# Kernel tuning notes

Measured on AMD Instinct MI355X. Metric: run time of the kernel, lower is better.

Reference implementation:

```python
import jax, jax.numpy as jnp
import numpy as np

B, C, T = 8, 128, 4096
H = C // 2  # 64


def setup_inputs() -> dict:
    key = jax.random.key(0)
    ks = jax.random.split(key, 9)
    s = 1.0 / np.sqrt(C)
    so = 1.0 / np.sqrt(H)
    return {
        "x": jax.random.normal(ks[0], (B, C, T), dtype=jnp.float32),
        "w_theta": jax.random.normal(ks[1], (H, C), dtype=jnp.float32) * s,
        "b_theta": jax.random.normal(ks[2], (H,), dtype=jnp.float32) * s,
        "w_phi": jax.random.normal(ks[3], (H, C), dtype=jnp.float32) * s,
        "b_phi": jax.random.normal(ks[4], (H,), dtype=jnp.float32) * s,
        "w_g": jax.random.normal(ks[5], (H, C), dtype=jnp.float32) * s,
        "b_g": jax.random.normal(ks[6], (H,), dtype=jnp.float32) * s,
        "w_out": jax.random.normal(ks[7], (C, H), dtype=jnp.float32) * so,
        "b_out": jax.random.normal(ks[8], (C,), dtype=jnp.float32) * so,
    }


def reference(x, w_theta, b_theta, w_phi, b_phi, w_g, b_g, w_out, b_out):
    # 1x1 conv == channel-mixing linear: [B,C,T] -> [B,H,T]
    theta = jnp.einsum("hc,bct->bht", w_theta, x) + b_theta[None, :, None]
    phi = jnp.einsum("hc,bct->bht", w_phi, x) + b_phi[None, :, None]
    g = jnp.einsum("hc,bct->bht", w_g, x) + b_g[None, :, None]
    # scores[b,t,s] = theta[b,:,t] . phi[b,:,s]; softmax over s (last dim)
    scores = jnp.einsum("bht,bhs->bts", theta, phi)  # [B,T,T]
    attn = jax.nn.softmax(scores, axis=-1)
    # out[b,h,t] = sum_s g[b,h,s] * attn[b,t,s]
    out = jnp.einsum("bhs,bts->bht", g, attn)  # [B,H,T]
    out = jnp.einsum("ch,bht->bct", w_out, out) + b_out[None, :, None]
    return x + out
```

## Files before the change

kernel.cpp:

```cpp
#include <hip/hip_runtime.h>
#include <hip/hip_bf16.h>

typedef _Float16 half_t;
typedef half_t halfx8 __attribute__((ext_vector_type(8)));
typedef half_t halfx4 __attribute__((ext_vector_type(4)));
typedef half_t halfx2 __attribute__((ext_vector_type(2)));
typedef __fp16 fp16x2 __attribute__((ext_vector_type(2)));
typedef float f32x4 __attribute__((ext_vector_type(4)));
typedef float f32x16 __attribute__((ext_vector_type(16)));
typedef int i32x4 __attribute__((ext_vector_type(4)));

#define B_ 8
#define C_ 128
#define T_ 4096
#define H_ 64
#define L2E 1.44269504088896340736f

static __device__ __forceinline__ halfx2 pk2(float a, float b) {
    fp16x2 r = __builtin_amdgcn_cvt_pkrtz(a, b);
    return __builtin_bit_cast(halfx2, r);
}
static __device__ __forceinline__ int pk2i(float a, float b) {
    return __builtin_bit_cast(int, __builtin_amdgcn_cvt_pkrtz(a, b));
}
static __device__ __forceinline__ float fast_exp2(float x) {
    return __builtin_amdgcn_exp2f(x);
}
static __device__ __forceinline__ float max3f(float a, float b, float c) {
    return fmaxf(fmaxf(a, b), c);
}
static __device__ __forceinline__ int swz(int row, int col) {
    return (row << 6) + (col ^ ((row & 7) << 3));
}
static __device__ __forceinline__ int swz4(int row, int col) {
    return (row << 6) + ((col & ~7) ^ ((row & 7) << 3)) + (col & 7);
}

__global__ __launch_bounds__(256) void proj_kernel(
    const float* __restrict__ x,
    const float* __restrict__ w_theta, const float* __restrict__ b_theta,
    const float* __restrict__ w_phi,   const float* __restrict__ b_phi,
    const float* __restrict__ w_g,     const float* __restrict__ b_g,
    half_t* __restrict__ Q, half_t* __restrict__ Ko, half_t* __restrict__ Vt)
{
    __shared__ __align__(16) half_t xt[64][136];
    __shared__ __align__(16) half_t ts[64][72];

    const int tid  = threadIdx.x;
    const int lane = tid & 63;
    const int wave = tid >> 6;
    const int b    = blockIdx.x >> 6;
    const int t0   = (blockIdx.x & 63) << 6;

    const int rowA  = lane & 15;
    const int kgrp  = lane >> 4;
    const int row_d = kgrp << 2;

    const float* xb = x + (size_t)b * C_ * T_ + t0;
    #pragma unroll
    for (int it = 0; it < 8; ++it) {
        int li = it * 256 + tid;
        int c  = li >> 4;
        int tc = li & 15;
        f32x4 v = *(const f32x4*)(xb + (size_t)c * T_ + tc * 4);
        #pragma unroll
        for (int j = 0; j < 4; ++j) xt[tc * 4 + j][c] = (half_t)v[j];
    }

    const int h0 = wave << 4;
    const float* Ws[3] = {w_theta, w_phi, w_g};
    const float* Bs[3] = {b_theta, b_phi, b_g};
    halfx8 wa[3][4];
    #pragma unroll
    for (int m = 0; m < 3; ++m) {
        const float* wrow = Ws[m] + (size_t)(h0 + rowA) * C_;
        #pragma unroll
        for (int cc = 0; cc < 4; ++cc) {
            const float* p = wrow + cc * 32 + kgrp * 8;
            f32x4 a = *(const f32x4*)p;
            f32x4 c2 = *(const f32x4*)(p + 4);
            halfx8 f;
            f[0]=(half_t)a[0]; f[1]=(half_t)a[1]; f[2]=(half_t)a[2]; f[3]=(half_t)a[3];
            f[4]=(half_t)c2[0];f[5]=(half_t)c2[1];f[6]=(half_t)c2[2];f[7]=(half_t)c2[3];
            wa[m][cc] = f;
        }
    }

    __syncthreads();

    #pragma unroll
    for (int m = 0; m < 3; ++m) {
        f32x4 acc[4] = {};
        #pragma unroll
        for (int tt = 0; tt < 4; ++tt) {
            #pragma unroll
            for (int cc = 0; cc < 4; ++cc) {
                halfx8 bfrag = *(const halfx8*)&xt[tt * 16 + rowA][cc * 32 + kgrp * 8];
                acc[tt] = __builtin_amdgcn_mfma_f32_16x16x32_f16(wa[m][cc], bfrag, acc[tt], 0, 0, 0);
            }
        }
        float bias[4];
        #pragma unroll
        for (int r = 0; r < 4; ++r) bias[r] = Bs[m][h0 + row_d + r];

        if (m < 2) {
            const float sc = (m == 0) ? L2E : 1.0f;
            #pragma unroll
            for (int tt = 0; tt < 4; ++tt)
                #pragma unroll
                for (int r = 0; r < 4; ++r)
                    ts[tt * 16 + rowA][h0 + row_d + r] = (half_t)((acc[tt][r] + bias[r]) * sc);
            __syncthreads();
            half_t* dst = (m == 0 ? Q : Ko) + ((size_t)b * T_ + t0) * H_;
            #pragma unroll
            for (int it = 0; it < 2; ++it) {
                int q = it * 256 + tid;
                int t = q >> 3, hc = q & 7;
                *(halfx8*)(dst + (size_t)t * H_ + hc * 8) = *(const halfx8*)&ts[t][hc * 8];
            }
            __syncthreads();
        } else {
            half_t* dst = Vt + (size_t)b * H_ * T_ + t0;
            #pragma unroll
            for (int tt = 0; tt < 4; ++tt)
                #pragma unroll
                for (int r = 0; r < 4; ++r)
                    dst[(size_t)(h0 + row_d + r) * T_ + tt * 16 + rowA] = (half_t)(acc[tt][r] + bias[r]);
        }
    }
}

__global__ __launch_bounds__(256, 4) void attn_kernel(
    const half_t* __restrict__ Q, const half_t* __restrict__ K,
    const half_t* __restrict__ Vt, half_t* __restrict__ Op,
    float* __restrict__ Mp, float* __restrict__ Lp, int NS)
{
    __shared__ __align__(16) half_t Ks[2][64 * 64];
    __shared__ __align__(16) half_t Vs[2][64 * 64];

    const int tid  = threadIdx.x;
    const int wave = tid >> 6;
    const int lane = tid & 63;
    const int qb   = blockIdx.x / NS;
    const int sp   = blockIdx.x - qb * NS;
    const int b    = qb >> 5;
    const int t0   = (qb & 31) << 7;
    const int q0   = t0 + wave * 32;
    const int lq   = lane & 31;
    const int hi   = lane >> 5;
    const int NT   = T_ / (64 * NS);
    const int sbase = sp * (T_ / NS);

    halfx8 qf[4];
    const half_t* qr = Q + ((size_t)b * T_ + q0 + lq) * H_ + hi * 8;
    #pragma unroll
    for (int kc = 0; kc < 4; ++kc) qf[kc] = *(const halfx8*)(qr + kc * 16);

    f32x16 oacc[2] = {};
    float mr = -INFINITY, lr = 0.f;

    const int r0 = tid >> 3;
    const int c8 = (tid & 7) * 8;
    const int gA = (c8 & ~15) + ((c8 & 8) >> 1);
    const half_t* kp = K  + (size_t)b * T_ * H_ + (size_t)(sbase + r0) * H_ + c8;
    const half_t* vp = Vt + (size_t)b * H_ * T_ + (size_t)r0 * T_ + sbase + c8;

    halfx8 rK0 = *(const halfx8*)kp;
    halfx8 rK1 = *(const halfx8*)(kp + 32 * H_);
    halfx8 rV0 = *(const halfx8*)vp;
    halfx8 rV1 = *(const halfx8*)(vp + 32 * T_);
    kp += 64 * H_; vp += 64;

    {
        *(halfx8*)&Ks[0][swz(r0, c8)]      = rK0;
        *(halfx8*)&Ks[0][swz(r0 + 32, c8)] = rK1;
        union { halfx8 h8; halfx4 h4[2]; } u0, u1;
        u0.h8 = rV0; u1.h8 = rV1;
        *(halfx4*)&Vs[0][swz4(r0, gA)]          = u0.h4[0];
        *(halfx4*)&Vs[0][swz4(r0, gA + 8)]      = u0.h4[1];
        *(halfx4*)&Vs[0][swz4(r0 + 32, gA)]     = u1.h4[0];
        *(halfx4*)&Vs[0][swz4(r0 + 32, gA + 8)] = u1.h4[1];
    }
    __syncthreads();

    for (int t = 0; t < NT; ++t) {
        const int cur = t & 1;
        const bool more = (t + 1 < NT);
        if (more) {
            rK0 = *(const halfx8*)kp;
            rK1 = *(const halfx8*)(kp + 32 * H_);
            rV0 = *(const halfx8*)vp;
            rV1 = *(const halfx8*)(vp + 32 * T_);
            kp += 64 * H_; vp += 64;
        }

        f32x16 sacc[2] = {};
        __builtin_amdgcn_s_setprio(1);
        #pragma unroll
        for (int st = 0; st < 2; ++st)
            #pragma unroll
            for (int kc = 0; kc < 4; ++kc) {
                halfx8 kf = *(const halfx8*)&Ks[cur][swz(st * 32 + lq, kc * 16 + hi * 8)];
                sacc[st] = __builtin_amdgcn_mfma_f32_32x32x16_f16(kf, qf[kc], sacc[st], 0, 0, 0);
            }
        __builtin_amdgcn_s_setprio(0);

        float pm;
        {
            float a0 = max3f(sacc[0][0],  sacc[0][1],  sacc[0][2]);
            float a1 = max3f(sacc[0][3],  sacc[0][4],  sacc[0][5]);
            float a2 = max3f(sacc[0][6],  sacc[0][7],  sacc[0][8]);
            float a3 = max3f(sacc[0][9],  sacc[0][10], sacc[0][11]);
            float a4 = max3f(sacc[0][12], sacc[0][13], sacc[0][14]);
            float b0 = max3f(sacc[1][0],  sacc[1][1],  sacc[1][2]);
            float b1 = max3f(sacc[1][3],  sacc[1][4],  sacc[1][5]);
            float b2 = max3f(sacc[1][6],  sacc[1][7],  sacc[1][8]);
            float b3 = max3f(sacc[1][9],  sacc[1][10], sacc[1][11]);
            float b4 = max3f(sacc[1][12], sacc[1][13], sacc[1][14]);
            float c0 = max3f(a0, a1, sacc[0][15]);
            float c1 = max3f(a2, a3, a4);
            float c2 = max3f(b0, b1, sacc[1][15]);
            float c3 = max3f(b2, b3, b4);
            pm = fmaxf(max3f(c0, c1, c2), c3);
        }
        if (__any(pm > mr + 8.f)) {
            pm = fmaxf(pm, __shfl_xor(pm, 32));
            float mnew  = fmaxf(mr, pm);
            float scale = fast_exp2(mr - mnew);
            mr = mnew; lr *= scale;
            #pragma unroll
            for (int dt = 0; dt < 2; ++dt)
                #pragma unroll
                for (int r = 0; r < 16; ++r) oacc[dt][r] *= scale;
        }
        float p0 = 0.f, p1 = 0.f, p2 = 0.f, p3 = 0.f;
        #pragma unroll
        for (int st = 0; st < 2; ++st) {
            #pragma unroll
            for (int r = 0; r < 16; r += 4) {
                float e0 = fast_exp2(sacc[st][r + 0] - mr);
                float e1 = fast_exp2(sacc[st][r + 1] - mr);
                float e2 = fast_exp2(sacc[st][r + 2] - mr);
                float e3 = fast_exp2(sacc[st][r + 3] - mr);
                sacc[st][r + 0] = e0; sacc[st][r + 1] = e1;
                sacc[st][r + 2] = e2; sacc[st][r + 3] = e3;
                p0 += e0; p1 += e1; p2 += e2; p3 += e3;
            }
        }
        float ps = (p0 + p1) + (p2 + p3);
        lr += ps + __shfl_xor(ps, 32);

        halfx8 pfrag[4];
        #pragma unroll
        for (int sc = 0; sc < 4; ++sc) {
            const int st = sc >> 1, rb = (sc & 1) * 8;
            i32x4 w;
            w[0] = pk2i(sacc[st][rb + 0], sacc[st][rb + 1]);
            w[1] = pk2i(sacc[st][rb + 2], sacc[st][rb + 3]);
            w[2] = pk2i(sacc[st][rb + 4], sacc[st][rb + 5]);
            w[3] = pk2i(sacc[st][rb + 6], sacc[st][rb + 7]);
            pfrag[sc] = __builtin_bit_cast(halfx8, w);
        }

        __builtin_amdgcn_s_setprio(1);
        #pragma unroll
        for (int sc = 0; sc < 4; ++sc) {
            halfx8 vf0 = *(const halfx8*)&Vs[cur][swz(lq,      sc * 16 + hi * 8)];
            halfx8 vf1 = *(const halfx8*)&Vs[cur][swz(32 + lq, sc * 16 + hi * 8)];
            oacc[0] = __builtin_amdgcn_mfma_f32_32x32x16_f16(vf0, pfrag[sc], oacc[0], 0, 0, 0);
            oacc[1] = __builtin_amdgcn_mfma_f32_32x32x16_f16(vf1, pfrag[sc], oacc[1], 0, 0, 0);
        }
        __builtin_amdgcn_s_setprio(0);

        if (more) {
            const int nxt = cur ^ 1;
            *(halfx8*)&Ks[nxt][swz(r0, c8)]      = rK0;
            *(halfx8*)&Ks[nxt][swz(r0 + 32, c8)] = rK1;
            union { halfx8 h8; halfx4 h4[2]; } u0, u1;
            u0.h8 = rV0; u1.h8 = rV1;
            *(halfx4*)&Vs[nxt][swz4(r0, gA)]          = u0.h4[0];
            *(halfx4*)&Vs[nxt][swz4(r0, gA + 8)]      = u0.h4[1];
            *(halfx4*)&Vs[nxt][swz4(r0 + 32, gA)]     = u1.h4[0];
            *(halfx4*)&Vs[nxt][swz4(r0 + 32, gA + 8)] = u1.h4[1];
            __syncthreads();
        }
    }

    const int BT = B_ * T_;
    const int grow = b * T_ + q0 + lq;
    float inv = 1.f / lr;
    half_t* od = Op + ((size_t)sp * BT + grow) * H_;
    #pragma unroll
    for (int dt = 0; dt < 2; ++dt)
        #pragma unroll
        for (int g = 0; g < 4; ++g) {
            union { halfx2 h2[2]; halfx4 h4; } u;
            u.h2[0] = pk2(oacc[dt][g * 4 + 0] * inv, oacc[dt][g * 4 + 1] * inv);
            u.h2[1] = pk2(oacc[dt][g * 4 + 2] * inv, oacc[dt][g * 4 + 3] * inv);
            *(halfx4*)(od + dt * 32 + g * 8 + hi * 4) = u.h4;
        }
    if (Mp != nullptr && hi == 0) {
        Mp[(size_t)sp * BT + grow] = mr;
        Lp[(size_t)sp * BT + grow] = lr;
    }
}

__global__ __launch_bounds__(256) void merge_kernel(
    const half_t* __restrict__ Op, const float* __restrict__ Mp,
    const float* __restrict__ Lp, half_t* __restrict__ O, int NS)
{
    const int idx = blockIdx.x * 256 + threadIdx.x;
    const int row = idx >> 3;
    const int hc  = (idx & 7) * 8;
    const int BT  = B_ * T_;

    float m = -INFINITY;
    for (int s = 0; s < NS; ++s) m = fmaxf(m, Mp[(size_t)s * BT + row]);
    float W = 0.f;
    float acc[8] = {};
    for (int s = 0; s < NS; ++s) {
        float w = Lp[(size_t)s * BT + row] * __builtin_amdgcn_exp2f(Mp[(size_t)s * BT + row] - m);
        W += w;
        halfx8 o = *(const halfx8*)(Op + ((size_t)s * BT + row) * H_ + hc);
        #pragma unroll
        for (int j = 0; j < 8; ++j) acc[j] += w * (float)o[j];
    }
    float inv = 1.f / W;
    halfx8 r;
    #pragma unroll
    for (int j = 0; j < 8; ++j) r[j] = (half_t)(acc[j] * inv);
    *(halfx8*)(O + (size_t)row * H_ + hc) = r;
}

__global__ __launch_bounds__(256) void outproj_kernel(
    const half_t* __restrict__ O, const float* __restrict__ w_out,
    const float* __restrict__ b_out, const float* __restrict__ x,
    float* __restrict__ out)
{
    __shared__ __align__(16) half_t Ot[64][72];

    const int tid  = threadIdx.x;
    const int lane = tid & 63;
    const int wave = tid >> 6;
    const int b    = blockIdx.x >> 6;
    const int t0   = (blockIdx.x & 63) << 6;

    const int rowA  = lane & 15;
    const int kgrp  = lane >> 4;
    const int row_d = kgrp << 2;

    #pragma unroll
    for (int it = 0; it < 2; ++it) {
        int q = it * 256 + tid;
        int t = q >> 3, hc = q & 7;
        *(halfx8*)&Ot[t][hc * 8] = *(const halfx8*)(O + ((size_t)b * T_ + t0 + t) * H_ + hc * 8);
    }

    const int c0 = wave * 32;
    halfx8 wf[2][2];
    #pragma unroll
    for (int ct = 0; ct < 2; ++ct) {
        const float* wrow = w_out + (size_t)(c0 + ct * 16 + rowA) * H_;
        #pragma unroll
        for (int hc = 0; hc < 2; ++hc) {
            const float* p = wrow + hc * 32 + kgrp * 8;
            f32x4 a = *(const f32x4*)p;
            f32x4 c2 = *(const f32x4*)(p + 4);
            halfx8 f;
            f[0]=(half_t)a[0]; f[1]=(half_t)a[1]; f[2]=(half_t)a[2]; f[3]=(half_t)a[3];
            f[4]=(half_t)c2[0];f[5]=(half_t)c2[1];f[6]=(half_t)c2[2];f[7]=(half_t)c2[3];
            wf[ct][hc] = f;
        }
    }

    __syncthreads();

    #pragma unroll
    for (int ct = 0; ct < 2; ++ct) {
        #pragma unroll
        for (int tt = 0; tt < 4; ++tt) {
            f32x4 acc = {};
            #pragma unroll
            for (int hc = 0; hc < 2; ++hc) {
                halfx8 of = *(const halfx8*)&Ot[tt * 16 + rowA][hc * 32 + kgrp * 8];
                acc = __builtin_amdgcn_mfma_f32_16x16x32_f16(wf[ct][hc], of, acc, 0, 0, 0);
            }
            const int c = c0 + ct * 16 + row_d;
            const size_t base = (size_t)b * C_ * T_ + t0 + tt * 16 + rowA;
            #pragma unroll
            for (int r = 0; r < 4; ++r) {
                size_t idx = base + (size_t)(c + r) * T_;
                out[idx] = x[idx] + b_out[c + r] + acc[r];
            }
        }
    }
}

extern "C" void kernel_launch(void* const* d_in, const int* in_sizes, int n_in,
                              void* d_out, int out_size, void* d_ws, size_t ws_size,
                              hipStream_t stream) {
    const float* x       = (const float*)d_in[0];
    const float* w_theta = (const float*)d_in[1];
    const float* b_theta = (const float*)d_in[2];
    const float* w_phi   = (const float*)d_in[3];
    const float* b_phi   = (const float*)d_in[4];
    const float* w_g     = (const float*)d_in[5];
    const float* b_g     = (const float*)d_in[6];
    const float* w_out   = (const float*)d_in[7];
    const float* b_out   = (const float*)d_in[8];
    float* out = (float*)d_out;

    const size_t mat = (size_t)B_ * T_ * H_;
    const size_t BT  = (size_t)B_ * T_;
    half_t* Qw = (half_t*)d_ws;
    half_t* Kw = Qw + mat;
    half_t* Vw = Kw + mat;
    half_t* Ow = Vw + mat;
    const size_t base_b = 4 * mat * sizeof(half_t);

    auto need = [&](size_t ns) { return base_b + ns * mat * 2 + ns * BT * 8; };
    const int NS = (ws_size >= need(4)) ? 4 : ((ws_size >= need(2)) ? 2 : 1);

    half_t* Opart = Ow;
    float*  Mp = nullptr;
    float*  Lp = nullptr;
    if (NS > 1) {
        Opart = (half_t*)((char*)d_ws + base_b);
        Mp = (float*)((char*)d_ws + base_b + (size_t)NS * mat * 2);
        Lp = Mp + (size_t)NS * BT;
    }

    proj_kernel<<<dim3(B_ * (T_ / 64)), dim3(256), 0, stream>>>(
        x, w_theta, b_theta, w_phi, b_phi, w_g, b_g, Qw, Kw, Vw);
    attn_kernel<<<dim3(B_ * (T_ / 128) * NS), dim3(256), 0, stream>>>(
        Qw, Kw, Vw, Opart, Mp, Lp, NS);
    if (NS > 1)
        merge_kernel<<<dim3((int)(BT * H_ / (256 * 8))), dim3(256), 0, stream>>>(
            Opart, Mp, Lp, Ow, NS);
    outproj_kernel<<<dim3(B_ * (T_ / 64)), dim3(256), 0, stream>>>(Ow, w_out, b_out, x, out);
}
```

Measured before the change: 77.41 us.

## Fuse split-KV merge into output projection and defer row-sum shuffle

The separate merge kernel that combines split-KV partial outputs is removed. That combine now runs inside the output-projection kernel while it loads its tile into shared memory, which saves a launch and a round trip of the merged O through global memory. The cross-half row-sum shuffle in the attention inner loop is also moved out to a single shuffle after the loop, cutting one cross-lane operation per iteration. The trade-off is that the outproj load phase does more scattered reads and some scalar math before its MFMA work.

```diff
diff --git a/kernel.cpp b/kernel.cpp
--- a/kernel.cpp
+++ b/kernel.cpp
@@ -247,8 +247,7 @@
                 p0 += e0; p1 += e1; p2 += e2; p3 += e3;
             }
         }
-        float ps = (p0 + p1) + (p2 + p3);
-        lr += ps + __shfl_xor(ps, 32);
+        lr += (p0 + p1) + (p2 + p3);
 
         halfx8 pfrag[4];
         #pragma unroll
@@ -288,7 +287,8 @@
 
     const int BT = B_ * T_;
     const int grow = b * T_ + q0 + lq;
-    float inv = 1.f / lr;
+    const float lrt = lr + __shfl_xor(lr, 32);
+    float inv = 1.f / lrt;
     half_t* od = Op + ((size_t)sp * BT + grow) * H_;
     #pragma unroll
     for (int dt = 0; dt < 2; ++dt)
@@ -301,41 +301,15 @@
         }
     if (Mp != nullptr && hi == 0) {
         Mp[(size_t)sp * BT + grow] = mr;
-        Lp[(size_t)sp * BT + grow] = lr;
-    }
-}
-
-__global__ __launch_bounds__(256) void merge_kernel(
+        Lp[(size_t)sp * BT + grow] = lrt;
+    }
+}
+
+__global__ __launch_bounds__(256) void outproj_kernel(
     const half_t* __restrict__ Op, const float* __restrict__ Mp,
-    const float* __restrict__ Lp, half_t* __restrict__ O, int NS)
-{
-    const int idx = blockIdx.x * 256 + threadIdx.x;
-    const int row = idx >> 3;
-    const int hc  = (idx & 7) * 8;
-    const int BT  = B_ * T_;
-
-    float m = -INFINITY;
-    for (int s = 0; s < NS; ++s) m = fmaxf(m, Mp[(size_t)s * BT + row]);
-    float W = 0.f;
-    float acc[8] = {};
-    for (int s = 0; s < NS; ++s) {
-        float w = Lp[(size_t)s * BT + row] * __builtin_amdgcn_exp2f(Mp[(size_t)s * BT + row] - m);
-        W += w;
-        halfx8 o = *(const halfx8*)(Op + ((size_t)s * BT + row) * H_ + hc);
-        #pragma unroll
-        for (int j = 0; j < 8; ++j) acc[j] += w * (float)o[j];
-    }
-    float inv = 1.f / W;
-    halfx8 r;
-    #pragma unroll
-    for (int j = 0; j < 8; ++j) r[j] = (half_t)(acc[j] * inv);
-    *(halfx8*)(O + (size_t)row * H_ + hc) = r;
-}
-
-__global__ __launch_bounds__(256) void outproj_kernel(
-    const half_t* __restrict__ O, const float* __restrict__ w_out,
-    const float* __restrict__ b_out, const float* __restrict__ x,
-    float* __restrict__ out)
+    const float* __restrict__ Lp, int NS,
+    const float* __restrict__ w_out, const float* __restrict__ b_out,
+    const float* __restrict__ x, float* __restrict__ out)
 {
     __shared__ __align__(16) half_t Ot[64][72];
 
@@ -348,12 +322,34 @@
     const int rowA  = lane & 15;
     const int kgrp  = lane >> 4;
     const int row_d = kgrp << 2;
+    const int BT    = B_ * T_;
 
     #pragma unroll
     for (int it = 0; it < 2; ++it) {
         int q = it * 256 + tid;
-        int t = q >> 3, hc = q & 7;
-        *(halfx8*)&Ot[t][hc * 8] = *(const halfx8*)(O + ((size_t)b * T_ + t0 + t) * H_ + hc * 8);
+        int t = q >> 3, hc = (q & 7) * 8;
+        const size_t row = (size_t)b * T_ + t0 + t;
+        if (Mp == nullptr) {
+            *(halfx8*)&Ot[t][hc] = *(const halfx8*)(Op + row * H_ + hc);
+        } else {
+            float m = Mp[row];
+            for (int s = 1; s < NS; ++s) m = fmaxf(m, Mp[(size_t)s * BT + row]);
+            float W = 0.f;
+            float acc[8] = {};
+            for (int s = 0; s < NS; ++s) {
+                float w = Lp[(size_t)s * BT + row] *
+                          __builtin_amdgcn_exp2f(Mp[(size_t)s * BT + row] - m);
+                W += w;
+                halfx8 o = *(const halfx8*)(Op + ((size_t)s * BT + row) * H_ + hc);
+                #pragma unroll
+                for (int j = 0; j < 8; ++j) acc[j] += w * (float)o[j];
+            }
+            float inv = 1.f / W;
+            halfx8 r;
+            #pragma unroll
+            for (int j = 0; j < 8; ++j) r[j] = (half_t)(acc[j] * inv);
+            *(halfx8*)&Ot[t][hc] = r;
+        }
     }
 
     const int c0 = wave * 32;
@@ -434,8 +430,6 @@
         x, w_theta, b_theta, w_phi, b_phi, w_g, b_g, Qw, Kw, Vw);
     attn_kernel<<<dim3(B_ * (T_ / 128) * NS), dim3(256), 0, stream>>>(
         Qw, Kw, Vw, Opart, Mp, Lp, NS);
-    if (NS > 1)
-        merge_kernel<<<dim3((int)(BT * H_ / (256 * 8))), dim3(256), 0, stream>>>(
-            Opart, Mp, Lp, Ow, NS);
-    outproj_kernel<<<dim3(B_ * (T_ / 64)), dim3(256), 0, stream>>>(Ow, w_out, b_out, x, out);
-}
+    outproj_kernel<<<dim3(B_ * (T_ / 64)), dim3(256), 0, stream>>>(
+        Opart, Mp, Lp, NS, w_out, b_out, x, out);
+}
```

After: 84.22 us. 1.09x slower.
